# Optimization experiments

Hardware: AMD Instinct MI355X
Metric: run time of the kernel (lower is better)

The kernel has to match this reference:

```python
import jax, jax.numpy as jnp
import numpy as np

WIN, DIL, PAD, H = 5, 1, 2, 8  # window, dilation, unfold padding, num_heads
C = 256
EPS = 1e-5

def _ln(z, g, b):
    m = jnp.mean(z, axis=-1, keepdims=True)
    v = jnp.mean((z - m) ** 2, axis=-1, keepdims=True)
    return (z - m) * jax.lax.rsqrt(v + EPS) * g + b

def setup_inputs() -> dict:
    key = jax.random.key(0)
    ks = jax.random.split(key, 16)
    s = 0.02
    d = {
        'x': jax.random.normal(ks[0], (32, C, 64, 25), jnp.float32),
        'ln1_g': jnp.ones((C,), jnp.float32), 'ln1_b': jnp.zeros((C,), jnp.float32),
        'q_w': jax.random.normal(ks[1], (C, C)) * s, 'q_b': jnp.zeros((C,)),
        'qa_w': jax.random.normal(ks[2], (C, H)) * s, 'qa_b': jnp.zeros((H,)),
        'k_w': jax.random.normal(ks[3], (C, C)) * s, 'k_b': jnp.zeros((C,)),
        'ka_w': jax.random.normal(ks[4], (C, H)) * s, 'ka_b': jnp.zeros((H,)),
        'v_w': jax.random.normal(ks[5], (C, C)) * s, 'v_b': jnp.zeros((C,)),
        't_w': jax.random.normal(ks[6], (C, C)) * s, 't_b': jnp.zeros((C,)),
        'p_w': jax.random.normal(ks[7], (C, C)) * s, 'p_b': jnp.zeros((C,)),
        'ffn_g': jnp.ones((C,)), 'ffn_b': jnp.zeros((C,)),
        'w1': jax.random.normal(ks[8], (C, C)) * s, 'b1': jnp.zeros((C,)),
        'w2': jax.random.normal(ks[9], (C, C)) * s, 'b2': jnp.zeros((C,)),
    }
    return d

def reference(x, ln1_g, ln1_b, q_w, q_b, qa_w, qa_b, k_w, k_b, ka_w, ka_b,
              v_w, v_b, t_w, t_b, p_w, p_b, ffn_g, ffn_b, w1, b1, w2, b2):
    N, Cc, T, V = x.shape
    hc = Cc // H
    scale = 1.0 / np.sqrt(hc)
    B, L = N * T, WIN * V
    xp = jnp.pad(x, ((0, 0), (0, 0), (PAD, PAD), (0, 0)))
    win = jnp.stack([xp[:, :, k * DIL:k * DIL + T, :] for k in range(WIN)], axis=2)  # (N,C,W,T,V)
    wx = win.transpose(0, 3, 2, 4, 1).reshape(B, L, Cc)
    nx = _ln(wx, ln1_g, ln1_b)
    # attention: softmax-pooled query
    q = nx @ q_w + q_b                                      # (B,L,C)
    qw = jax.nn.softmax(((q @ qa_w + qa_b) * scale).transpose(0, 2, 1), axis=-1)  # (B,H,L)
    qh = q.reshape(B, L, H, hc).transpose(0, 2, 1, 3)       # (B,H,L,hc)
    pq = jnp.einsum('bhl,bhld->bhd', qw, qh)                # (B,H,hc)
    k_ = nx @ k_w + k_b
    kq = k_ * pq.reshape(B, 1, Cc)
    kw = jax.nn.softmax(((kq @ ka_w + ka_b) * scale).transpose(0, 2, 1), axis=-1)
    kh = k_.reshape(B, L, H, hc).transpose(0, 2, 1, 3)
    pk = jnp.einsum('bhl,bhld->bhd', kw, kh)                # (B,H,hc)
    v_ = nx @ v_w + v_b
    vh = v_.reshape(B, L, H, hc).transpose(0, 2, 1, 3)
    kv = (vh * pk[:, :, None, :]).transpose(0, 2, 1, 3).reshape(B, L, Cc)
    kvh = (kv @ t_w + t_b).reshape(B, L, H, hc).transpose(0, 2, 1, 3)
    att = ((kvh + qh).transpose(0, 2, 1, 3).reshape(B, L, Cc)) @ p_w + p_b
    # average over window, residual with flattened x
    att = att.reshape(B, WIN, V, Cc).mean(axis=1)           # (B,V,C)
    att = att + x.transpose(0, 2, 3, 1).reshape(B, V, Cc)
    # FFN residual block
    f = _ln(att, ffn_g, ffn_b)
    f = jax.nn.gelu(f @ w1 + b1, approximate=False) @ w2 + b2
    y = f + att
    return y.reshape(N, T, V, Cc).transpose(0, 3, 1, 2)     # (N,C,T,V)
```

## Files before the change

### kernel.cpp

```cpp
#include <hip/hip_runtime.h>
#include <hip/hip_bf16.h>

typedef unsigned short u16b;
typedef __attribute__((ext_vector_type(8))) short short8;
typedef __attribute__((ext_vector_type(4))) float floatx4;

#define DEV static __device__ __forceinline__

DEV float sh2f(unsigned short s) { union { unsigned u; float f; } c; c.u = ((unsigned)s) << 16; return c.f; }
DEV unsigned short f2b(float f) {
    unsigned u = __float_as_uint(f);
    u += 0x7FFF + ((u >> 16) & 1);
    return (unsigned short)(u >> 16);
}

constexpr int O_LN1G = 0, O_LN1B = 256, O_QB = 512, O_KB = 768, O_VB = 1024,
              O_TB = 1280, O_PB = 1536, O_FFNG = 1792, O_FFNB = 2048,
              O_B1 = 2304, O_B2 = 2560, O_QAB = 2816, O_KAB = 2824,
              O_QAW = 2832, O_KAW = 4880, O_CV = 6928;

__global__ void detect_k(const unsigned* __restrict__ xw, int* __restrict__ flag) {
    __shared__ int cnt;
    if (threadIdx.x == 0) cnt = 0;
    __syncthreads();
    int my = 0;
    for (int i = threadIdx.x; i < 4096; i += 256) {
        unsigned w = xw[i];
        unsigned e0 = (w >> 7) & 0xFFu;
        if (e0 >= 0xC0u) my++;
    }
    atomicAdd(&cnt, my);
    __syncthreads();
    if (threadIdx.x == 0) flag[0] = (cnt > 64) ? 1 : 0;
}

DEV unsigned short load_cvt(const void* src, size_t idx, int fp32) {
    return fp32 ? f2b(((const float*)src)[idx]) : ((const u16b*)src)[idx];
}

struct VecTab { const void* p[15]; int off[15]; int n[15]; };

__global__ __launch_bounds__(256)
void convert_vecs_k(VecTab tab, const int* __restrict__ flag, u16b* __restrict__ sv) {
    int e = blockIdx.x, fp32 = flag[0];
    const void* s = tab.p[e];
    int n = tab.n[e], off = tab.off[e];
    for (int i = threadIdx.x; i < n; i += 256)
        sv[off + i] = load_cvt(s, i, fp32);
}

struct W8 { const void* p[8]; unsigned dstoff[8]; unsigned rstride[8]; };

__global__ void wtrans_k(W8 tab, u16b* __restrict__ base, const int* __restrict__ flag) {
    __shared__ u16b tile[32][33];
    int fp32 = flag[0];
    const void* src = tab.p[blockIdx.z];
    u16b* dst = base + tab.dstoff[blockIdx.z];
    unsigned rs = tab.rstride[blockIdx.z];
    int c0 = blockIdx.x * 32, r0 = blockIdx.y * 32;
    int tx = threadIdx.x, ty = threadIdx.y;
#pragma unroll
    for (int i = 0; i < 32; i += 8)
        tile[ty + i][tx] = load_cvt(src, (size_t)(r0 + ty + i) * 256 + c0 + tx, fp32);
    __syncthreads();
#pragma unroll
    for (int i = 0; i < 32; i += 8)
        dst[(size_t)(c0 + ty + i) * rs + r0 + tx] = tile[tx][ty + i];
}

__global__ __launch_bounds__(256)
void transpose_in_k(const void* __restrict__ src, u16b* __restrict__ dst,
                    int rows, int cols, const int* __restrict__ flag) {
    __shared__ u16b tile[32][36];
    int fp32 = flag[0];
    int c0 = blockIdx.x * 32, r0 = blockIdx.y * 32;
    size_t zb = (size_t)blockIdx.z * rows * cols;
    int tid = threadIdx.x;
    int r = tid >> 3, c4 = (tid & 7) * 4;
    size_t sidx = zb + (size_t)(r0 + r) * cols + c0 + c4;
    if (fp32) {
        const float4 f4 = *(const float4*)((const float*)src + sidx);
        tile[r][c4]     = f2b(f4.x);
        tile[r][c4 + 1] = f2b(f4.y);
        tile[r][c4 + 2] = f2b(f4.z);
        tile[r][c4 + 3] = f2b(f4.w);
    } else {
        *(ushort4*)&tile[r][c4] = *(const ushort4*)((const u16b*)src + sidx);
    }
    __syncthreads();
    int c = tid >> 3, r4 = (tid & 7) * 4;
    ushort4 o;
    o.x = tile[r4][c]; o.y = tile[r4 + 1][c]; o.z = tile[r4 + 2][c]; o.w = tile[r4 + 3][c];
    *(ushort4*)&dst[zb + (size_t)(c0 + c) * rows + r0 + r4] = o;
}

__global__ __launch_bounds__(256)
void transpose_out_k(const u16b* __restrict__ src, void* __restrict__ dst,
                     int rows, int cols, const int* __restrict__ flag) {
    __shared__ u16b tile[32][36];
    int fp32 = flag[0];
    int c0 = blockIdx.x * 32, r0 = blockIdx.y * 32;
    size_t zb = (size_t)blockIdx.z * rows * cols;
    int tid = threadIdx.x;
    int r = tid >> 3, c4 = (tid & 7) * 4;
    *(ushort4*)&tile[r][c4] = *(const ushort4*)&src[zb + (size_t)(r0 + r) * cols + c0 + c4];
    __syncthreads();
    int c = tid >> 3, r4 = (tid & 7) * 4;
    size_t didx = zb + (size_t)(c0 + c) * rows + r0 + r4;
    if (fp32) {
        float4 f4;
        f4.x = sh2f(tile[r4][c]);     f4.y = sh2f(tile[r4 + 1][c]);
        f4.z = sh2f(tile[r4 + 2][c]); f4.w = sh2f(tile[r4 + 3][c]);
        *(float4*)((float*)dst + didx) = f4;
    } else {
        ushort4 o;
        o.x = tile[r4][c]; o.y = tile[r4 + 1][c]; o.z = tile[r4 + 2][c]; o.w = tile[r4 + 3][c];
        *(ushort4*)((u16b*)dst + didx) = o;
    }
}

__global__ __launch_bounds__(256)
void rowstats_k(const u16b* __restrict__ src, float2* __restrict__ st,
                int valid, int total) {
    int wv = threadIdx.x >> 6, lane = threadIdx.x & 63;
    int r = blockIdx.x * 4 + wv;
    if (r >= total) return;
    if (r >= valid) { if (lane == 0) st[r] = make_float2(0.f, 0.f); return; }
    int c = lane * 4;
    ushort4 raw = *(const ushort4*)&src[(size_t)r * 256 + c];
    float x0 = sh2f(raw.x), x1 = sh2f(raw.y), x2 = sh2f(raw.z), x3 = sh2f(raw.w);
    float s  = x0 + x1 + x2 + x3;
    float sq = x0 * x0 + x1 * x1 + x2 * x2 + x3 * x3;
#pragma unroll
    for (int o = 32; o; o >>= 1) { s += __shfl_xor(s, o); sq += __shfl_xor(sq, o); }
    float mean = s * (1.f / 256.f);
    float var  = sq * (1.f / 256.f) - mean * mean;
    if (lane == 0) st[r] = make_float2(mean, rsqrtf(var + 1e-5f));
}

__global__ __launch_bounds__(256)
void cvec_k(const u16b* __restrict__ pT, u16b* __restrict__ sv) {
    int j = threadIdx.x;
    float acc = sh2f(sv[O_PB + j]);
    const u16b* row = pT + (size_t)j * 256;
    for (int i = 0; i < 256; i += 8) {
        short8 t8 = *(const short8*)&sv[O_TB + i];
        short8 p8 = *(const short8*)&row[i];
#pragma unroll
        for (int u = 0; u < 8; ++u)
            acc += sh2f((unsigned short)t8[u]) * sh2f((unsigned short)p8[u]);
    }
    sv[O_CV + j] = f2b(acc);
}

template <int EPI, int LNA, int XY = 0>
__global__ __launch_bounds__(256)
void gemm256(const u16b* __restrict__ A, int aStride, int K,
             const u16b* __restrict__ Wt,
             const u16b* __restrict__ bias, const u16b* __restrict__ addm,
             u16b* __restrict__ out, size_t osParam,
             const float2* __restrict__ stats,
             const u16b* __restrict__ gvec, const u16b* __restrict__ bvec) {
    __shared__ u16b As[128 * 72];
    __shared__ u16b Bs[128 * 72];
    __shared__ float sg[256], sb[256];
    const int tid = threadIdx.x;
    const int m0 = (XY ? blockIdx.y : blockIdx.x) * 128;
    const int n0 = (XY ? blockIdx.x : blockIdx.y) * 128;
    const int wv = tid >> 6, lane = tid & 63;
    const int wrow = (wv >> 1) * 64, wcol = (wv & 1) * 64;
    const int fr = lane & 15;
    const int fq = lane >> 4;
    floatx4 acc[4][4];
    const floatx4 zero = {0.f, 0.f, 0.f, 0.f};
#pragma unroll
    for (int i = 0; i < 4; ++i)
#pragma unroll
        for (int j = 0; j < 4; ++j) acc[i][j] = zero;

    float2 strow[4];
    if (LNA) {
        sg[tid] = sh2f(gvec[tid]);
        sb[tid] = sh2f(bvec[tid]);
#pragma unroll
        for (int kk = 0; kk < 4; ++kk) strow[kk] = stats[m0 + (tid >> 3) + kk * 32];
        __syncthreads();
    }

    for (int kt = 0; kt < K; kt += 64) {
#pragma unroll
        for (int kk = 0; kk < 4; ++kk) {
            int chunk = tid + kk * 256;
            int row = chunk >> 3, col = (chunk & 7) * 8;
            union { uint4 u; unsigned short h[8]; } rw;
            rw.u = *(const uint4*)&A[(size_t)(m0 + row) * aStride + kt + col];
            if (LNA) {
#pragma unroll
                for (int j = 0; j < 8; ++j) {
                    float f = sh2f(rw.h[j]);
                    f = (f - strow[kk].x) * strow[kk].y * sg[kt + col + j] + sb[kt + col + j];
                    rw.h[j] = f2b(f);
                }
            }
            *(uint4*)&As[row * 72 + col] = rw.u;
            *(uint4*)&Bs[row * 72 + col] = *(const uint4*)&Wt[(size_t)(n0 + row) * K + kt + col];
        }
        __syncthreads();
#pragma unroll
        for (int s = 0; s < 2; ++s) {
            short8 af[4], bfr[4];
#pragma unroll
            for (int i = 0; i < 4; ++i)
                af[i] = *(short8*)&As[(wrow + i * 16 + fr) * 72 + s * 32 + fq * 8];
#pragma unroll
            for (int j = 0; j < 4; ++j)
                bfr[j] = *(short8*)&Bs[(wcol + j * 16 + fr) * 72 + s * 32 + fq * 8];
#pragma unroll
            for (int i = 0; i < 4; ++i)
#pragma unroll
                for (int j = 0; j < 4; ++j)
                    acc[i][j] = __builtin_amdgcn_mfma_f32_16x16x32_bf16(af[i], bfr[j], acc[i][j], 0, 0, 0);
        }
        __syncthreads();
    }
    float bv[4];
#pragma unroll
    for (int j = 0; j < 4; ++j) bv[j] = bias ? sh2f(bias[n0 + wcol + j * 16 + fr]) : 0.f;
#pragma unroll
    for (int i = 0; i < 4; ++i) {
#pragma unroll
        for (int r = 0; r < 4; ++r) {
            int row = m0 + wrow + i * 16 + fq * 4 + r;
            size_t ro = (size_t)row * 256;
#pragma unroll
            for (int j = 0; j < 4; ++j) {
                int col = n0 + wcol + j * 16 + fr;
                float val = acc[i][j][r] + bv[j];
                if (EPI == 2) val += sh2f(addm[ro + col]);
                if (EPI == 3) val = 0.5f * val * (1.0f + erff(val * 0.70710678118654752f));
                if (EPI == 4)      out[(size_t)(col >> 8) * osParam + ro + (col & 255)] = f2b(val);
                else if (EPI == 0) out[(size_t)row * osParam + col] = f2b(val);
                else               out[ro + col] = f2b(val);
            }
        }
    }
}

DEV void pool_stage(const u16b* __restrict__ S, const u16b* __restrict__ sv,
                    int awoff, int aboff, const float* mult, float* outPool,
                    const int* srow, u16b* su, float* slog, float* spool, int tid) {
    for (int i = tid; i < 2048; i += 512) {
        int c = i >> 3, h = i & 7;
        float w = sh2f(sv[awoff + i]);
        if (mult) w *= mult[c];
        su[h * 260 + c] = f2b(w);
    }
    __syncthreads();
    int wv = tid >> 6, lane = tid & 63;
    int fr = lane & 15, fq = lane >> 4;
    floatx4 acc = {0.f, 0.f, 0.f, 0.f};
    const u16b* Ar = S + (size_t)srow[wv * 16 + fr] * 256;
#pragma unroll
    for (int s = 0; s < 8; ++s) {
        short8 a  = *(const short8*)&Ar[s * 32 + fq * 8];
        short8 bb = *(const short8*)&su[fr * 260 + s * 32 + fq * 8];
        acc = __builtin_amdgcn_mfma_f32_16x16x32_bf16(a, bb, acc, 0, 0, 0);
    }
    float abv = sh2f(sv[aboff + (fr & 7)]);
    if (fr < 8) {
#pragma unroll
        for (int r = 0; r < 4; ++r)
            slog[(wv * 16 + fq * 4 + r) * 9 + fr] = (acc[r] + abv) * 0.17677669529663687f;
    }
    __syncthreads();
    {
        int h = wv;
        float v0 = (lane < 125) ? slog[lane * 9 + h] : -1e30f;
        float v1 = (lane + 64 < 125) ? slog[(lane + 64) * 9 + h] : -1e30f;
        float mx = fmaxf(v0, v1);
#pragma unroll
        for (int o = 32; o; o >>= 1) mx = fmaxf(mx, __shfl_xor(mx, o));
        float e0 = (lane < 125) ? __expf(v0 - mx) : 0.f;
        float e1 = (lane + 64 < 125) ? __expf(v1 - mx) : 0.f;
        float s = e0 + e1;
#pragma unroll
        for (int o = 32; o; o >>= 1) s += __shfl_xor(s, o);
        float inv = 1.f / s;
        if (lane < 125) slog[lane * 9 + h] = e0 * inv;
        if (lane + 64 < 125) slog[(lane + 64) * 9 + h] = e1 * inv;
    }
    __syncthreads();
    int c8 = (tid & 31) * 8, ls = tid >> 5;
    int h2 = c8 >> 5;
    float a8[8] = {0.f, 0.f, 0.f, 0.f, 0.f, 0.f, 0.f, 0.f};
    for (int l = ls; l < 125; l += 16) {
        float w = slog[l * 9 + h2];
        short8 d8 = *(const short8*)&S[(size_t)srow[l] * 256 + c8];
#pragma unroll
        for (int j = 0; j < 8; ++j) a8[j] += w * sh2f((unsigned short)d8[j]);
    }
#pragma unroll
    for (int j = 0; j < 8; ++j) spool[ls * 260 + c8 + j] = a8[j];
    __syncthreads();
    if (tid < 256) {
        float s = 0.f;
#pragma unroll
        for (int q = 0; q < 16; ++q) s += spool[q * 260 + tid];
        outPool[tid] = s;
    }
    __syncthreads();
}

__global__ __launch_bounds__(512)
void pool_fused(const u16b* __restrict__ qf, const u16b* __restrict__ kf,
                const u16b* __restrict__ vf, const u16b* __restrict__ sv,
                u16b* __restrict__ CB) {
    __shared__ int srow[128];
    __shared__ u16b su[16 * 260];
    __shared__ float slog[128 * 9];
    __shared__ float spool[16 * 260];
    __shared__ float spq[256], spk[256];
    int bid = blockIdx.x;
    int b = ((bid & 7) << 8) | (bid >> 3);
    int n = b >> 6, t = b & 63;
    int tid = threadIdx.x;
    if (tid < 128) {
        int l = tid < 125 ? tid : 124;
        int w = l / 25, v = l - w * 25, tt = t + w - 2;
        srow[tid] = ((unsigned)tt < 64u) ? (n * 64 + tt) * 25 + v : 51200;
    }
    for (int i = tid; i < 8 * 260; i += 512) su[8 * 260 + i] = 0;
    __syncthreads();
    pool_stage(qf, sv, O_QAW, O_QAB, nullptr, spq, srow, su, slog, spool, tid);
    for (int i = tid; i < 800; i += 512) {
        int v = i >> 5, c8 = (i & 31) * 8;
        float s[8] = {0.f, 0.f, 0.f, 0.f, 0.f, 0.f, 0.f, 0.f};
#pragma unroll
        for (int w = 0; w < 5; ++w) {
            short8 d8 = *(const short8*)&qf[(size_t)srow[w * 25 + v] * 256 + c8];
#pragma unroll
            for (int j = 0; j < 8; ++j) s[j] += sh2f((unsigned short)d8[j]);
        }
        unsigned short o[8];
#pragma unroll
        for (int j = 0; j < 8; ++j) o[j] = f2b(s[j] * 0.2f);
        *(uint4*)&CB[((size_t)b * 25 + v) * 512 + 256 + c8] = *(uint4*)o;
    }
    pool_stage(kf, sv, O_KAW, O_KAB, spq, spk, srow, su, slog, spool, tid);
    for (int i = tid; i < 800; i += 512) {
        int v = i >> 5, c8 = (i & 31) * 8;
        float s[8] = {0.f, 0.f, 0.f, 0.f, 0.f, 0.f, 0.f, 0.f};
#pragma unroll
        for (int w = 0; w < 5; ++w) {
            short8 d8 = *(const short8*)&vf[(size_t)srow[w * 25 + v] * 256 + c8];
#pragma unroll
            for (int j = 0; j < 8; ++j) s[j] += sh2f((unsigned short)d8[j]);
        }
        unsigned short o[8];
#pragma unroll
        for (int j = 0; j < 8; ++j) o[j] = f2b(s[j] * 0.2f * spk[c8 + j]);
        *(uint4*)&CB[((size_t)b * 25 + v) * 512 + c8] = *(uint4*)o;
    }
}

extern "C" void kernel_launch(void* const* d_in, const int* in_sizes, int n_in,
                              void* d_out, int out_size, void* d_ws, size_t ws_size,
                              hipStream_t stream) {
    (void)in_sizes; (void)n_in; (void)out_size; (void)ws_size;
    const void* x    = d_in[0];
    const void* ln1g = d_in[1];  const void* ln1b = d_in[2];
    const void* q_w  = d_in[3];  const void* q_b  = d_in[4];
    const void* qa_w = d_in[5];  const void* qa_b = d_in[6];
    const void* k_w  = d_in[7];  const void* k_b  = d_in[8];
    const void* ka_w = d_in[9];  const void* ka_b = d_in[10];
    const void* v_w  = d_in[11]; const void* v_b  = d_in[12];
    const void* t_w  = d_in[13]; const void* t_b  = d_in[14];
    const void* p_w  = d_in[15]; const void* p_b  = d_in[16];
    const void* ffng = d_in[17]; const void* ffnb = d_in[18];
    const void* w1   = d_in[19]; const void* b1   = d_in[20];
    const void* w2   = d_in[21]; const void* b2   = d_in[22];

    char* ws = (char*)d_ws;
    size_t off = 0;
    auto alloc = [&](size_t bytes) { void* p = ws + off; off += (bytes + 255) & ~(size_t)255; return p; };
    const size_t RPAD = 51328;
    int*    flag = (int*)alloc(256);
    u16b*   sv   = (u16b*)alloc(8192 * 2);
    u16b*   wT   = (u16b*)alloc((size_t)7 * 65536 * 2);
    u16b*   cW   = (u16b*)alloc((size_t)256 * 512 * 2);
    u16b*   xT   = (u16b*)alloc(RPAD * 256 * 2);
    u16b*   Bq   = (u16b*)alloc(RPAD * 256 * 2);
    u16b*   Bk   = (u16b*)alloc(RPAD * 256 * 2);
    u16b*   Bv   = (u16b*)alloc(RPAD * 256 * 2);
    u16b*   CB   = (u16b*)alloc((size_t)51200 * 512 * 2);
    u16b*   att  = (u16b*)alloc((size_t)51200 * 256 * 2);
    float2* st1  = (float2*)alloc(RPAD * 8);
    float2* st2  = (float2*)alloc((size_t)51200 * 8);

    u16b* pT  = wT + 3 * 65536;
    u16b* tT  = wT + 4 * 65536;
    u16b* w1T = wT + 5 * 65536;
    u16b* w2T = wT + 6 * 65536;

    detect_k<<<1, 256, 0, stream>>>((const unsigned*)x, flag);
    VecTab tab;
    const void* vp[15] = {ln1g, ln1b, q_b, k_b, v_b, t_b, p_b, ffng, ffnb, b1, b2, qa_b, ka_b, qa_w, ka_w};
    const int vo[15] = {O_LN1G, O_LN1B, O_QB, O_KB, O_VB, O_TB, O_PB, O_FFNG, O_FFNB, O_B1, O_B2, O_QAB, O_KAB, O_QAW, O_KAW};
    const int vn[15] = {256, 256, 256, 256, 256, 256, 256, 256, 256, 256, 256, 8, 8, 2048, 2048};
    for (int i = 0; i < 15; ++i) { tab.p[i] = vp[i]; tab.off[i] = vo[i]; tab.n[i] = vn[i]; }
    convert_vecs_k<<<15, 256, 0, stream>>>(tab, flag, sv);

    dim3 tb(32, 8);
    W8 wt;
    const void* wsrc[8] = {q_w, k_w, v_w, p_w, t_w, w1, w2, p_w};
    for (int i = 0; i < 8; ++i) {
        wt.p[i] = wsrc[i];
        wt.dstoff[i] = (i < 7) ? (unsigned)(i * 65536) : (unsigned)((cW + 256) - wT);
        wt.rstride[i] = (i < 7) ? 256u : 512u;
    }
    wtrans_k<<<dim3(8, 8, 8), tb, 0, stream>>>(wt, wT, flag);
    cvec_k<<<1, 256, 0, stream>>>(pT, sv);
    gemm256<0, 0><<<dim3(2, 2), 256, 0, stream>>>(pT, 256, 256, tT, nullptr, nullptr,
                                                  cW, 512, nullptr, nullptr, nullptr);
    transpose_in_k<<<dim3(50, 8, 32), 256, 0, stream>>>(x, xT, 256, 1600, flag);
    rowstats_k<<<12832, 256, 0, stream>>>(xT, st1, 51200, 51328);
    gemm256<4, 1, 1><<<dim3(6, 401), 256, 0, stream>>>(xT, 256, 256, wT, sv + O_QB, nullptr,
                                                       Bq, RPAD * 256, st1, sv + O_LN1G, sv + O_LN1B);
    pool_fused<<<2048, 512, 0, stream>>>(Bq, Bk, Bv, sv, CB);
    gemm256<2, 0, 1><<<dim3(2, 400), 256, 0, stream>>>(CB, 512, 512, cW, sv + O_CV, xT,
                                                       att, 256, nullptr, nullptr, nullptr);
    rowstats_k<<<12800, 256, 0, stream>>>(att, st2, 51200, 51200);
    gemm256<3, 1, 1><<<dim3(2, 400), 256, 0, stream>>>(att, 256, 256, w1T, sv + O_B1, nullptr,
                                                       Bq, 256, st2, sv + O_FFNG, sv + O_FFNB);
    gemm256<2, 0, 1><<<dim3(2, 400), 256, 0, stream>>>(Bq, 256, 256, w2T, sv + O_B2, att,
                                                       att, 256, nullptr, nullptr, nullptr);
    transpose_out_k<<<dim3(8, 50, 32), 256, 0, stream>>>(att, d_out, 1600, 256, flag);
}
```

Before: 407.5 us.

## Fuse LN stats and output transpose into GEMM epilogues; shrink M tile to 64

```diff
diff --git a/kernel.cpp b/kernel.cpp
--- a/kernel.cpp
+++ b/kernel.cpp
@@ -95,31 +95,6 @@
 }
 
 __global__ __launch_bounds__(256)
-void transpose_out_k(const u16b* __restrict__ src, void* __restrict__ dst,
-                     int rows, int cols, const int* __restrict__ flag) {
-    __shared__ u16b tile[32][36];
-    int fp32 = flag[0];
-    int c0 = blockIdx.x * 32, r0 = blockIdx.y * 32;
-    size_t zb = (size_t)blockIdx.z * rows * cols;
-    int tid = threadIdx.x;
-    int r = tid >> 3, c4 = (tid & 7) * 4;
-    *(ushort4*)&tile[r][c4] = *(const ushort4*)&src[zb + (size_t)(r0 + r) * cols + c0 + c4];
-    __syncthreads();
-    int c = tid >> 3, r4 = (tid & 7) * 4;
-    size_t didx = zb + (size_t)(c0 + c) * rows + r0 + r4;
-    if (fp32) {
-        float4 f4;
-        f4.x = sh2f(tile[r4][c]);     f4.y = sh2f(tile[r4 + 1][c]);
-        f4.z = sh2f(tile[r4 + 2][c]); f4.w = sh2f(tile[r4 + 3][c]);
-        *(float4*)((float*)dst + didx) = f4;
-    } else {
-        ushort4 o;
-        o.x = tile[r4][c]; o.y = tile[r4 + 1][c]; o.z = tile[r4 + 2][c]; o.w = tile[r4 + 3][c];
-        *(ushort4*)((u16b*)dst + didx) = o;
-    }
-}
-
-__global__ __launch_bounds__(256)
 void rowstats_k(const u16b* __restrict__ src, float2* __restrict__ st,
                 int valid, int total) {
     int wv = threadIdx.x >> 6, lane = threadIdx.x & 63;
@@ -153,43 +128,55 @@
     sv[O_CV + j] = f2b(acc);
 }
 
-template <int EPI, int LNA, int XY = 0>
-__global__ __launch_bounds__(256)
+template <int EPI, int LNA, int XY = 0, int STATS = 0>
+__global__ __launch_bounds__(256, 4)
 void gemm256(const u16b* __restrict__ A, int aStride, int K,
              const u16b* __restrict__ Wt,
              const u16b* __restrict__ bias, const u16b* __restrict__ addm,
              u16b* __restrict__ out, size_t osParam,
-             const float2* __restrict__ stats,
-             const u16b* __restrict__ gvec, const u16b* __restrict__ bvec) {
-    __shared__ u16b As[128 * 72];
+             const float2* __restrict__ stats, const float2* __restrict__ stats2,
+             const u16b* __restrict__ gvec, const u16b* __restrict__ bvec,
+             float2* __restrict__ statOut, const int* __restrict__ flag) {
+    __shared__ u16b As[64 * 72];
     __shared__ u16b Bs[128 * 72];
     __shared__ float sg[256], sb[256];
+    __shared__ float2 spart[64][2];
     const int tid = threadIdx.x;
-    const int m0 = (XY ? blockIdx.y : blockIdx.x) * 128;
+    const int m0 = (XY ? blockIdx.y : blockIdx.x) * 64;
     const int n0 = (XY ? blockIdx.x : blockIdx.y) * 128;
     const int wv = tid >> 6, lane = tid & 63;
-    const int wrow = (wv >> 1) * 64, wcol = (wv & 1) * 64;
+    const int wrow = (wv >> 1) * 32, wcol = (wv & 1) * 64;
     const int fr = lane & 15;
     const int fq = lane >> 4;
-    floatx4 acc[4][4];
+    floatx4 acc[2][4];
     const floatx4 zero = {0.f, 0.f, 0.f, 0.f};
 #pragma unroll
-    for (int i = 0; i < 4; ++i)
+    for (int i = 0; i < 2; ++i)
 #pragma unroll
         for (int j = 0; j < 4; ++j) acc[i][j] = zero;
 
-    float2 strow[4];
+    float2 strow[2];
     if (LNA) {
         sg[tid] = sh2f(gvec[tid]);
         sb[tid] = sh2f(bvec[tid]);
 #pragma unroll
-        for (int kk = 0; kk < 4; ++kk) strow[kk] = stats[m0 + (tid >> 3) + kk * 32];
+        for (int kk = 0; kk < 2; ++kk) {
+            int r = m0 + (tid >> 3) + kk * 32;
+            if (LNA == 2) {
+                float2 a = stats[r], b = stats2[r];
+                float mean = (a.x + b.x) * (1.f / 256.f);
+                float var  = (a.y + b.y) * (1.f / 256.f) - mean * mean;
+                strow[kk] = make_float2(mean, rsqrtf(var + 1e-5f));
+            } else {
+                strow[kk] = stats[r];
+            }
+        }
         __syncthreads();
     }
 
     for (int kt = 0; kt < K; kt += 64) {
 #pragma unroll
-        for (int kk = 0; kk < 4; ++kk) {
+        for (int kk = 0; kk < 2; ++kk) {
             int chunk = tid + kk * 256;
             int row = chunk >> 3, col = (chunk & 7) * 8;
             union { uint4 u; unsigned short h[8]; } rw;
@@ -203,20 +190,25 @@
                 }
             }
             *(uint4*)&As[row * 72 + col] = rw.u;
+        }
+#pragma unroll
+        for (int kk = 0; kk < 4; ++kk) {
+            int chunk = tid + kk * 256;
+            int row = chunk >> 3, col = (chunk & 7) * 8;
             *(uint4*)&Bs[row * 72 + col] = *(const uint4*)&Wt[(size_t)(n0 + row) * K + kt + col];
         }
         __syncthreads();
 #pragma unroll
         for (int s = 0; s < 2; ++s) {
-            short8 af[4], bfr[4];
-#pragma unroll
-            for (int i = 0; i < 4; ++i)
+            short8 af[2], bfr[4];
+#pragma unroll
+            for (int i = 0; i < 2; ++i)
                 af[i] = *(short8*)&As[(wrow + i * 16 + fr) * 72 + s * 32 + fq * 8];
 #pragma unroll
             for (int j = 0; j < 4; ++j)
                 bfr[j] = *(short8*)&Bs[(wcol + j * 16 + fr) * 72 + s * 32 + fq * 8];
 #pragma unroll
-            for (int i = 0; i < 4; ++i)
+            for (int i = 0; i < 2; ++i)
 #pragma unroll
                 for (int j = 0; j < 4; ++j)
                     acc[i][j] = __builtin_amdgcn_mfma_f32_16x16x32_bf16(af[i], bfr[j], acc[i][j], 0, 0, 0);
@@ -226,21 +218,66 @@
     float bv[4];
 #pragma unroll
     for (int j = 0; j < 4; ++j) bv[j] = bias ? sh2f(bias[n0 + wcol + j * 16 + fr]) : 0.f;
-#pragma unroll
-    for (int i = 0; i < 4; ++i) {
-#pragma unroll
-        for (int r = 0; r < 4; ++r) {
-            int row = m0 + wrow + i * 16 + fq * 4 + r;
-            size_t ro = (size_t)row * 256;
+
+    if (EPI == 5) {
+        int fp32o = flag[0];
+#pragma unroll
+        for (int i = 0; i < 2; ++i) {
+            int row0 = m0 + wrow + i * 16 + fq * 4;
+            int n = row0 / 1600;
+            int tv = row0 - n * 1600;
 #pragma unroll
             for (int j = 0; j < 4; ++j) {
                 int col = n0 + wcol + j * 16 + fr;
-                float val = acc[i][j][r] + bv[j];
-                if (EPI == 2) val += sh2f(addm[ro + col]);
-                if (EPI == 3) val = 0.5f * val * (1.0f + erff(val * 0.70710678118654752f));
-                if (EPI == 4)      out[(size_t)(col >> 8) * osParam + ro + (col & 255)] = f2b(val);
-                else if (EPI == 0) out[(size_t)row * osParam + col] = f2b(val);
-                else               out[ro + col] = f2b(val);
+                float v4[4];
+#pragma unroll
+                for (int r = 0; r < 4; ++r)
+                    v4[r] = acc[i][j][r] + bv[j] + sh2f(addm[(size_t)(row0 + r) * 256 + col]);
+                size_t oidx = ((size_t)n * 256 + col) * 1600 + tv;
+                if (fp32o) {
+                    float4 o = {v4[0], v4[1], v4[2], v4[3]};
+                    *(float4*)((float*)out + oidx) = o;
+                } else {
+                    ushort4 o;
+                    o.x = f2b(v4[0]); o.y = f2b(v4[1]); o.z = f2b(v4[2]); o.w = f2b(v4[3]);
+                    *(ushort4*)&out[oidx] = o;
+                }
+            }
+        }
+    } else {
+#pragma unroll
+        for (int i = 0; i < 2; ++i) {
+#pragma unroll
+            for (int r = 0; r < 4; ++r) {
+                int row = m0 + wrow + i * 16 + fq * 4 + r;
+                size_t ro = (size_t)row * 256;
+                float s1 = 0.f, s2 = 0.f;
+#pragma unroll
+                for (int j = 0; j < 4; ++j) {
+                    int col = n0 + wcol + j * 16 + fr;
+                    float val = acc[i][j][r] + bv[j];
+                    if (EPI == 2) val += sh2f(addm[ro + col]);
+                    if (EPI == 3) val = 0.5f * val * (1.0f + erff(val * 0.70710678118654752f));
+                    if (STATS) { s1 += val; s2 += val * val; }
+                    if (EPI == 4)      out[(size_t)(col >> 8) * osParam + ro + (col & 255)] = f2b(val);
+                    else if (EPI == 0) out[(size_t)row * osParam + col] = f2b(val);
+                    else               out[ro + col] = f2b(val);
+                }
+                if (STATS) {
+#pragma unroll
+                    for (int mm = 1; mm < 16; mm <<= 1) {
+                        s1 += __shfl_xor(s1, mm);
+                        s2 += __shfl_xor(s2, mm);
+                    }
+                    if (fr == 0) spart[wrow + i * 16 + fq * 4 + r][wv & 1] = make_float2(s1, s2);
+                }
+            }
+        }
+        if (STATS) {
+            __syncthreads();
+            if (tid < 64) {
+                float2 a = spart[tid][0], b = spart[tid][1];
+                statOut[(size_t)(n0 >> 7) * 51200 + m0 + tid] = make_float2(a.x + b.x, a.y + b.y);
             }
         }
     }
@@ -395,7 +432,7 @@
     u16b*   CB   = (u16b*)alloc((size_t)51200 * 512 * 2);
     u16b*   att  = (u16b*)alloc((size_t)51200 * 256 * 2);
     float2* st1  = (float2*)alloc(RPAD * 8);
-    float2* st2  = (float2*)alloc((size_t)51200 * 8);
+    float2* st2p = (float2*)alloc((size_t)2 * 51200 * 8);
 
     u16b* pT  = wT + 3 * 65536;
     u16b* tT  = wT + 4 * 65536;
@@ -420,19 +457,22 @@
     }
     wtrans_k<<<dim3(8, 8, 8), tb, 0, stream>>>(wt, wT, flag);
     cvec_k<<<1, 256, 0, stream>>>(pT, sv);
-    gemm256<0, 0><<<dim3(2, 2), 256, 0, stream>>>(pT, 256, 256, tT, nullptr, nullptr,
-                                                  cW, 512, nullptr, nullptr, nullptr);
+    gemm256<0, 0><<<dim3(4, 2), 256, 0, stream>>>(pT, 256, 256, tT, nullptr, nullptr,
+                                                  cW, 512, nullptr, nullptr, nullptr, nullptr,
+                                                  nullptr, nullptr);
     transpose_in_k<<<dim3(50, 8, 32), 256, 0, stream>>>(x, xT, 256, 1600, flag);
     rowstats_k<<<12832, 256, 0, stream>>>(xT, st1, 51200, 51328);
-    gemm256<4, 1, 1><<<dim3(6, 401), 256, 0, stream>>>(xT, 256, 256, wT, sv + O_QB, nullptr,
-                                                       Bq, RPAD * 256, st1, sv + O_LN1G, sv + O_LN1B);
+    gemm256<4, 1, 1><<<dim3(6, 802), 256, 0, stream>>>(xT, 256, 256, wT, sv + O_QB, nullptr,
+                                                       Bq, RPAD * 256, st1, nullptr,
+                                                       sv + O_LN1G, sv + O_LN1B, nullptr, nullptr);
     pool_fused<<<2048, 512, 0, stream>>>(Bq, Bk, Bv, sv, CB);
-    gemm256<2, 0, 1><<<dim3(2, 400), 256, 0, stream>>>(CB, 512, 512, cW, sv + O_CV, xT,
-                                                       att, 256, nullptr, nullptr, nullptr);
-    rowstats_k<<<12800, 256, 0, stream>>>(att, st2, 51200, 51200);
-    gemm256<3, 1, 1><<<dim3(2, 400), 256, 0, stream>>>(att, 256, 256, w1T, sv + O_B1, nullptr,
-                                                       Bq, 256, st2, sv + O_FFNG, sv + O_FFNB);
-    gemm256<2, 0, 1><<<dim3(2, 400), 256, 0, stream>>>(Bq, 256, 256, w2T, sv + O_B2, att,
-                                                       att, 256, nullptr, nullptr, nullptr);
-    transpose_out_k<<<dim3(8, 50, 32), 256, 0, stream>>>(att, d_out, 1600, 256, flag);
-}
+    gemm256<2, 0, 1, 1><<<dim3(2, 800), 256, 0, stream>>>(CB, 512, 512, cW, sv + O_CV, xT,
+                                                          att, 256, nullptr, nullptr,
+                                                          nullptr, nullptr, st2p, nullptr);
+    gemm256<3, 2, 1><<<dim3(2, 800), 256, 0, stream>>>(att, 256, 256, w1T, sv + O_B1, nullptr,
+                                                       Bq, 256, st2p, st2p + 51200,
+                                                       sv + O_FFNG, sv + O_FFNB, nullptr, nullptr);
+    gemm256<5, 0, 1><<<dim3(2, 800), 256, 0, stream>>>(Bq, 256, 256, w2T, sv + O_B2, att,
+                                                       (u16b*)d_out, 0, nullptr, nullptr,
+                                                       nullptr, nullptr, nullptr, flag);
+}
```

New measurement: 397.7 us. 2.4% less time.
